# Performance work log

Measured on AMD Instinct MI355X. Metric: run time of the kernel, lower is better.

The kernel has to match this reference:

```python
import jax, jax.numpy as jnp
import numpy as np

B, N, D_IN, D_ATT = 8, 2048, 512, 512


def setup_inputs() -> dict:
    key = jax.random.key(0)
    ks = jax.random.split(key, 7)
    s_in = 1.0 / np.sqrt(D_IN)
    return {
        "x": jax.random.normal(ks[0], (B, N, D_IN), dtype=jnp.float32),
        "Wq": jax.random.uniform(ks[1], (D_IN, D_ATT), jnp.float32, -s_in, s_in),
        "bq": jax.random.uniform(ks[2], (D_ATT,), jnp.float32, -s_in, s_in),
        "Wk": jax.random.uniform(ks[3], (D_IN, D_ATT), jnp.float32, -s_in, s_in),
        "bk": jax.random.uniform(ks[4], (D_ATT,), jnp.float32, -s_in, s_in),
        "Wv": jax.random.uniform(ks[5], (D_IN, D_ATT), jnp.float32, -s_in, s_in),
        "bv": jax.random.uniform(ks[6], (D_ATT,), jnp.float32, -s_in, s_in),
    }


def reference(x, Wq, bq, Wk, bk, Wv, bv):
    # QKV projections: [B, N, D_ATT]
    Q = jnp.einsum("bnd,de->bne", x, Wq) + bq
    K = jnp.einsum("bnd,de->bne", x, Wk) + bk
    V = jnp.einsum("bnd,de->bne", x, Wv) + bv
    scale = 1.0 / jnp.sqrt(jnp.asarray(Q.shape[-1], Q.dtype))
    # scores[b, i, j] = Q[b,i] . K[b,j]  -> [B, N, N]
    scores = jnp.einsum("bie,bje->bij", Q, K) * scale
    # NOTE: original uses nn.Softmax(dim=1) -> normalize over the FIRST seq axis (queries)
    weights = jax.nn.softmax(scores, axis=1)
    out = jnp.einsum("bij,bje->bie", weights, V)
    return (out, weights)
```

## Files before the change

### kernel.cpp

```cpp
#include <hip/hip_runtime.h>
#include <hip/hip_bf16.h>
#include <stdint.h>

#define BB 8
#define NN 2048
#define DD 512

typedef unsigned short u16;
typedef __attribute__((ext_vector_type(8))) short bf16x8;
typedef __attribute__((ext_vector_type(8))) unsigned short u16x8;
typedef __attribute__((ext_vector_type(4))) float f32x4;

__device__ __forceinline__ float b2f(u16 h) {
  unsigned int u = ((unsigned int)h) << 16;
  float f;
  __builtin_memcpy(&f, &u, 4);
  return f;
}
__device__ __forceinline__ u16 f2b(float f) {
  unsigned int u;
  __builtin_memcpy(&u, &f, 4);
  u += 0x7fffu + ((u >> 16) & 1u);
  return (u16)(u >> 16);
}

__device__ __forceinline__ void glds16(const u16* g, u16* l) {
  __builtin_amdgcn_global_load_lds(
      (const __attribute__((address_space(1))) unsigned int*)g,
      (__attribute__((address_space(3))) unsigned int*)l, 16, 0, 0);
}

__global__ __launch_bounds__(256, 3)
void gemm_qkv(const u16* __restrict__ xb, const u16* __restrict__ WT,
              const float* __restrict__ bq, const float* __restrict__ bk,
              const float* __restrict__ bv,
              u16* __restrict__ Qb, u16* __restrict__ Kb, u16* __restrict__ VTb)
{
  __shared__ __align__(16) u16 sA[128 * 64];
  __shared__ __align__(16) u16 sB[128 * 64];
  const int tid  = threadIdx.x;
  const int wave = tid >> 6;
  const int lane = tid & 63;
  const int m0 = blockIdx.y * 128;
  const int n0 = blockIdx.x * 128;

  const int srow = wave * 8 + (lane >> 3);
  const int scol = (lane & 7) * 8;
  const u16* gA = xb + (long long)(m0 + srow) * 512 + scol;
  const u16* gB = WT + (long long)(n0 + srow) * 512 + scol;
  u16* lA = sA + wave * 512;
  u16* lB = sB + wave * 512;

  f32x4 acc[4][4];
#pragma unroll
  for (int i = 0; i < 4; ++i)
#pragma unroll
    for (int j = 0; j < 4; ++j) {
      f32x4 z = {0.f, 0.f, 0.f, 0.f};
      acc[i][j] = z;
    }

  const int wm  = (wave & 1) * 64;
  const int wn  = (wave >> 1) * 64;
  const int l15 = lane & 15;
  const int qk  = (lane >> 4) * 8;

  for (int k0 = 0; k0 < 512; k0 += 64) {
#pragma unroll
    for (int r = 0; r < 4; ++r) {
      glds16(gA + (long long)(r * 32) * 512 + k0, lA + r * 2048);
      glds16(gB + (long long)(r * 32) * 512 + k0, lB + r * 2048);
    }
    __syncthreads();
#pragma unroll
    for (int kk = 0; kk < 64; kk += 32) {
      bf16x8 af[4], bg[4];
#pragma unroll
      for (int mt = 0; mt < 4; ++mt)
        af[mt] = *(const bf16x8*)(sA + (wm + mt * 16 + l15) * 64 + kk + qk);
#pragma unroll
      for (int nt = 0; nt < 4; ++nt)
        bg[nt] = *(const bf16x8*)(sB + (wn + nt * 16 + l15) * 64 + kk + qk);
#pragma unroll
      for (int mt = 0; mt < 4; ++mt)
#pragma unroll
        for (int nt = 0; nt < 4; ++nt)
          acc[mt][nt] = __builtin_amdgcn_mfma_f32_16x16x32_bf16(
              af[mt], bg[nt], acc[mt][nt], 0, 0, 0);
    }
    __syncthreads();
  }

  const int rowq = (lane >> 4) * 4;
  const int route = n0 >> 9;
  const float* bp = (route == 0) ? bq : (route == 1) ? bk : bv;
#pragma unroll
  for (int nt = 0; nt < 4; ++nt) {
    const int gn = n0 + wn + nt * 16 + l15;
    const int ln = gn & 511;
    const float bval = bp[ln];
#pragma unroll
    for (int mt = 0; mt < 4; ++mt) {
      const int gm = m0 + wm + mt * 16 + rowq;
      if (route == 2) {
        const int b = gm >> 11;
        const int i = gm & (NN - 1);
        ushort4 pk;
        pk.x = f2b(acc[mt][nt][0] + bval);
        pk.y = f2b(acc[mt][nt][1] + bval);
        pk.z = f2b(acc[mt][nt][2] + bval);
        pk.w = f2b(acc[mt][nt][3] + bval);
        *(ushort4*)(&VTb[((long long)b * DD + ln) * NN + i]) = pk;
      } else {
        u16* Cb = (route == 0) ? Qb : Kb;
#pragma unroll
        for (int r = 0; r < 4; ++r)
          Cb[(long long)(gm + r) * DD + ln] = f2b(acc[mt][nt][r] + bval);
      }
    }
  }
}

__global__ __launch_bounds__(256, 3)
void gemm_s(const u16* __restrict__ Qb, const u16* __restrict__ Kb,
            u16* __restrict__ Eb, float* __restrict__ pl, float alpha)
{
  __shared__ __align__(16) u16 sA[128 * 64];
  __shared__ __align__(16) u16 sB[128 * 64];
  const int tid  = threadIdx.x;
  const int wave = tid >> 6;
  const int lane = tid & 63;
  const int m0 = blockIdx.y * 128;
  const int n0 = blockIdx.x * 128;
  const long long bz = blockIdx.z;
  const u16* A  = Qb + bz * (long long)NN * DD;
  const u16* Bt = Kb + bz * (long long)NN * DD;
  u16* E = Eb + bz * (long long)NN * NN;

  const int srow = wave * 8 + (lane >> 3);
  const int scol = (lane & 7) * 8;
  const u16* gA = A  + (long long)(m0 + srow) * DD + scol;
  const u16* gB = Bt + (long long)(n0 + srow) * DD + scol;
  u16* lA = sA + wave * 512;
  u16* lB = sB + wave * 512;

  f32x4 acc[4][4];
#pragma unroll
  for (int i = 0; i < 4; ++i)
#pragma unroll
    for (int j = 0; j < 4; ++j) {
      f32x4 z = {0.f, 0.f, 0.f, 0.f};
      acc[i][j] = z;
    }

  const int wm  = (wave & 1) * 64;
  const int wn  = (wave >> 1) * 64;
  const int l15 = lane & 15;
  const int qk  = (lane >> 4) * 8;

  for (int k0 = 0; k0 < DD; k0 += 64) {
#pragma unroll
    for (int r = 0; r < 4; ++r) {
      glds16(gA + (long long)(r * 32) * DD + k0, lA + r * 2048);
      glds16(gB + (long long)(r * 32) * DD + k0, lB + r * 2048);
    }
    __syncthreads();
#pragma unroll
    for (int kk = 0; kk < 64; kk += 32) {
      bf16x8 af[4], bg[4];
#pragma unroll
      for (int mt = 0; mt < 4; ++mt)
        af[mt] = *(const bf16x8*)(sA + (wm + mt * 16 + l15) * 64 + kk + qk);
#pragma unroll
      for (int nt = 0; nt < 4; ++nt)
        bg[nt] = *(const bf16x8*)(sB + (wn + nt * 16 + l15) * 64 + kk + qk);
#pragma unroll
      for (int mt = 0; mt < 4; ++mt)
#pragma unroll
        for (int nt = 0; nt < 4; ++nt)
          acc[mt][nt] = __builtin_amdgcn_mfma_f32_16x16x32_bf16(
              af[mt], bg[nt], acc[mt][nt], 0, 0, 0);
    }
    __syncthreads();
  }

  const int rowq = (lane >> 4) * 4;
  float coll[4];
#pragma unroll
  for (int nt = 0; nt < 4; ++nt) {
    float e[16];
#pragma unroll
    for (int mt = 0; mt < 4; ++mt)
#pragma unroll
      for (int r = 0; r < 4; ++r)
        e[mt * 4 + r] = __expf(fminf(acc[mt][nt][r] * alpha, 30.f));
    float sum = 0.f;
#pragma unroll
    for (int k = 0; k < 16; ++k) sum += e[k];
    sum += __shfl_xor(sum, 16);
    sum += __shfl_xor(sum, 32);
    coll[nt] = sum;
    const int gn = n0 + wn + nt * 16 + l15;
#pragma unroll
    for (int mt = 0; mt < 4; ++mt)
#pragma unroll
      for (int r = 0; r < 4; ++r)
        E[(long long)(m0 + wm + mt * 16 + rowq + r) * NN + gn] = f2b(e[mt * 4 + r]);
  }

  float* sred = (float*)sA;
  if (lane < 16) {
#pragma unroll
    for (int nt = 0; nt < 4; ++nt) {
      const int col = wn + nt * 16 + l15;
      sred[col * 2 + (wave & 1)] = coll[nt];
    }
  }
  __syncthreads();
  if (tid < 128) {
    const long long o = ((long long)bz * 16 + blockIdx.y) * NN + n0 + tid;
    pl[o] = sred[tid * 2] + sred[tid * 2 + 1];
  }
}

__global__ __launch_bounds__(256, 3)
void gemm_pv(const u16* __restrict__ A, const u16* __restrict__ Bt,
             float* __restrict__ C, int N, int K,
             long long sAb, long long sBb, long long sCb)
{
  __shared__ __align__(16) u16 sA[128 * 64];
  __shared__ __align__(16) u16 sB[128 * 64];
  const int tid  = threadIdx.x;
  const int wave = tid >> 6;
  const int lane = tid & 63;
  const int m0 = blockIdx.y * 128;
  const int n0 = blockIdx.x * 128;
  const long long bz = blockIdx.z;
  A  += bz * sAb;
  Bt += bz * sBb;
  C  += bz * sCb;

  const int srow = wave * 8 + (lane >> 3);
  const int scol = (lane & 7) * 8;
  const u16* gA = A  + (long long)(m0 + srow) * K + scol;
  const u16* gB = Bt + (long long)(n0 + srow) * K + scol;
  u16* lA = sA + wave * 512;
  u16* lB = sB + wave * 512;

  f32x4 acc[4][4];
#pragma unroll
  for (int i = 0; i < 4; ++i)
#pragma unroll
    for (int j = 0; j < 4; ++j) {
      f32x4 z = {0.f, 0.f, 0.f, 0.f};
      acc[i][j] = z;
    }

  const int wm  = (wave & 1) * 64;
  const int wn  = (wave >> 1) * 64;
  const int l15 = lane & 15;
  const int qk  = (lane >> 4) * 8;

  for (int k0 = 0; k0 < K; k0 += 64) {
#pragma unroll
    for (int r = 0; r < 4; ++r) {
      glds16(gA + (long long)(r * 32) * K + k0, lA + r * 2048);
      glds16(gB + (long long)(r * 32) * K + k0, lB + r * 2048);
    }
    __syncthreads();
#pragma unroll
    for (int kk = 0; kk < 64; kk += 32) {
      bf16x8 af[4], bg[4];
#pragma unroll
      for (int mt = 0; mt < 4; ++mt)
        af[mt] = *(const bf16x8*)(sA + (wm + mt * 16 + l15) * 64 + kk + qk);
#pragma unroll
      for (int nt = 0; nt < 4; ++nt)
        bg[nt] = *(const bf16x8*)(sB + (wn + nt * 16 + l15) * 64 + kk + qk);
#pragma unroll
      for (int mt = 0; mt < 4; ++mt)
#pragma unroll
        for (int nt = 0; nt < 4; ++nt)
          acc[mt][nt] = __builtin_amdgcn_mfma_f32_16x16x32_bf16(
              af[mt], bg[nt], acc[mt][nt], 0, 0, 0);
    }
    __syncthreads();
  }

  const int rowq = (lane >> 4) * 4;
#pragma unroll
  for (int nt = 0; nt < 4; ++nt) {
    const int gn = n0 + wn + nt * 16 + l15;
#pragma unroll
    for (int mt = 0; mt < 4; ++mt) {
#pragma unroll
      for (int r = 0; r < 4; ++r) {
        const int gm = m0 + wm + mt * 16 + rowq + r;
        C[(long long)gm * N + gn] = acc[mt][nt][r];
      }
    }
  }
}

__global__ __launch_bounds__(256)
void prep_inputs(const float* __restrict__ x, u16* __restrict__ xb,
                 const float* __restrict__ w0, const float* __restrict__ w1,
                 const float* __restrict__ w2, u16* __restrict__ WT)
{
  __shared__ float tile[64][65];
  const int bx = blockIdx.x;
  if (bx < 8192) {
    const long long i = ((long long)bx * 256 + threadIdx.x) * 4;
    const float4 v = *(const float4*)(x + i);
    ushort4 o;
    o.x = f2b(v.x); o.y = f2b(v.y); o.z = f2b(v.z); o.w = f2b(v.w);
    *(ushort4*)(xb + i) = o;
    return;
  }
  const int t = bx - 8192;
  const int z = t >> 6;
  const int s = t & 63;
  const float* in = (z == 0) ? w0 : (z == 1) ? w1 : w2;
  u16* o = WT + (long long)z * 512 * 512;
  const int r0 = (s >> 3) * 64;
  const int c0 = (s & 7) * 64;
  const int tr = threadIdx.x >> 6;
  const int tc = threadIdx.x & 63;
#pragma unroll
  for (int k = 0; k < 16; ++k) {
    const int r = k * 4 + tr;
    tile[r][tc] = in[(long long)(r0 + r) * 512 + c0 + tc];
  }
  __syncthreads();
#pragma unroll
  for (int k = 0; k < 16; ++k) {
    const int r = k * 4 + tr;
    o[(long long)(c0 + r) * 512 + r0 + tc] = f2b(tile[tc][r]);
  }
}

__global__ __launch_bounds__(256)
void softmax_combine(const float* __restrict__ pl, float* __restrict__ ec)
{
  const int idx = blockIdx.x * 256 + threadIdx.x;
  const int b = idx >> 11;
  const int j = idx & (NN - 1);
  const float* bl = pl + (long long)b * 16 * NN + j;
  float l = 0.f;
#pragma unroll
  for (int t = 0; t < 16; ++t)
    l += bl[(long long)t * NN];
  ec[idx] = 1.0f / l;
}

__global__ __launch_bounds__(256)
void vscale(u16* __restrict__ VTb, const float* __restrict__ ec)
{
  const long long idx = ((long long)blockIdx.x * 256 + threadIdx.x) * 8;
  const int b  = (int)(idx >> 20);
  const int j0 = (int)(idx & (NN - 1));
  const float* e = ec + b * NN + j0;
  u16x8 v = *(const u16x8*)(VTb + idx);
  u16x8 o;
#pragma unroll
  for (int k = 0; k < 8; ++k) o[k] = f2b(b2f(v[k]) * e[k]);
  *(u16x8*)(VTb + idx) = o;
}

__global__ __launch_bounds__(256)
void softmax_normalize(const u16* __restrict__ Eb, float* __restrict__ Wf,
                       const float* __restrict__ ec)
{
  const long long idx = ((long long)blockIdx.x * 256 + threadIdx.x) * 8;
  const int b  = (int)(idx >> 22);
  const int j0 = (int)(idx & (NN - 1));
  const float* e = ec + b * NN + j0;
  u16x8 v = *(const u16x8*)(Eb + idx);
  float w[8];
#pragma unroll
  for (int k = 0; k < 8; ++k)
    w[k] = b2f(v[k]) * e[k];
  float4 o0 = {w[0], w[1], w[2], w[3]};
  float4 o1 = {w[4], w[5], w[6], w[7]};
  *(float4*)(Wf + idx)     = o0;
  *(float4*)(Wf + idx + 4) = o1;
}

extern "C" void kernel_launch(void* const* d_in, const int* in_sizes, int n_in,
                              void* d_out, int out_size, void* d_ws, size_t ws_size,
                              hipStream_t stream)
{
  const float* x  = (const float*)d_in[0];
  const float* Wq = (const float*)d_in[1];
  const float* bq = (const float*)d_in[2];
  const float* Wk = (const float*)d_in[3];
  const float* bk = (const float*)d_in[4];
  const float* Wv = (const float*)d_in[5];
  const float* bv = (const float*)d_in[6];

  float* outf = (float*)d_out;
  float* Wf   = outf + (long long)BB * NN * DD;

  u16* Qb = (u16*)d_out;
  u16* Kb = Qb + (long long)BB * NN * DD;

  u16* Eb  = (u16*)d_ws;
  u16* spare = Eb + (long long)BB * NN * NN;
  u16* VTb = spare + (long long)BB * NN * NN;
  u16* xb  = VTb + (long long)BB * NN * DD;
  u16* WT  = xb + (long long)BB * NN * DD;
  float* pl  = (float*)(WT + 1536 * 512);
  float* ec  = pl + (long long)8 * 16 * NN;

  dim3 blk(256);

  prep_inputs<<<dim3(8192 + 192), blk, 0, stream>>>(x, xb, Wq, Wk, Wv, WT);

  gemm_qkv<<<dim3(12, 128), blk, 0, stream>>>(xb, WT, bq, bk, bv, Qb, Kb, VTb);

  const float scale = 0.044194173824159216f;
  gemm_s<<<dim3(16, 16, 8), blk, 0, stream>>>(Qb, Kb, Eb, pl, scale);

  softmax_combine<<<dim3(64), blk, 0, stream>>>(pl, ec);
  vscale<<<dim3(4096), blk, 0, stream>>>(VTb, ec);
  softmax_normalize<<<dim3(16384), blk, 0, stream>>>(Eb, Wf, ec);

  gemm_pv<<<dim3(4, 16, 8), blk, 0, stream>>>(Eb, VTb, outf, DD, NN,
      (long long)NN * NN, (long long)DD * NN, (long long)NN * DD);
}
```

Before: 363.0 us.

## Merge softmax normalization into PV GEMM launch as extra blocks

Removes the separate softmax_normalize kernel and folds its work into the PV GEMM launch. The grid grows from 4 to 12 blocks in x: the first 4 do the GEMM and the other 8 each normalize 32768 bf16 weights into the fp32 output. The memory-bound normalize can then run alongside the compute-bound GEMM and one launch is saved. In exchange, the GEMM blocks compete with the streaming blocks for bandwidth and CU slots, and both still read the same Eb buffer.

```diff
diff --git a/kernel.cpp b/kernel.cpp
--- a/kernel.cpp
+++ b/kernel.cpp
@@ -224,26 +224,51 @@
 }
 
 __global__ __launch_bounds__(256, 3)
-void gemm_pv(const u16* __restrict__ A, const u16* __restrict__ Bt,
-             float* __restrict__ C, int N, int K,
-             long long sAb, long long sBb, long long sCb)
+void gemm_pv_norm(const u16* __restrict__ A, const u16* __restrict__ Bt,
+                  float* __restrict__ C, float* __restrict__ Wf,
+                  const float* __restrict__ ec, int N, int K,
+                  long long sAb, long long sBb, long long sCb)
 {
   __shared__ __align__(16) u16 sA[128 * 64];
   __shared__ __align__(16) u16 sB[128 * 64];
-  const int tid  = threadIdx.x;
+  const int bx  = blockIdx.x;
+  const int tid = threadIdx.x;
+
+  if (bx >= 4) {
+    const int nb = (bx - 4) + 8 * (blockIdx.y + 16 * (int)blockIdx.z);
+    const long long base = (long long)nb * 32768;
+#pragma unroll
+    for (int it = 0; it < 16; ++it) {
+      const long long idx = base + it * 2048 + tid * 8;
+      const int b  = (int)(idx >> 22);
+      const int j0 = (int)(idx & (NN - 1));
+      const float* c = ec + b * NN + j0;
+      u16x8 v = *(const u16x8*)(A + idx);
+      float w[8];
+#pragma unroll
+      for (int k = 0; k < 8; ++k)
+        w[k] = b2f(v[k]) * c[k];
+      float4 o0 = {w[0], w[1], w[2], w[3]};
+      float4 o1 = {w[4], w[5], w[6], w[7]};
+      *(float4*)(Wf + idx)     = o0;
+      *(float4*)(Wf + idx + 4) = o1;
+    }
+    return;
+  }
+
   const int wave = tid >> 6;
   const int lane = tid & 63;
   const int m0 = blockIdx.y * 128;
-  const int n0 = blockIdx.x * 128;
+  const int n0 = bx * 128;
   const long long bz = blockIdx.z;
-  A  += bz * sAb;
-  Bt += bz * sBb;
-  C  += bz * sCb;
+  const u16* Ab  = A  + bz * sAb;
+  const u16* Btb = Bt + bz * sBb;
+  float* Cb      = C  + bz * sCb;
 
   const int srow = wave * 8 + (lane >> 3);
   const int scol = (lane & 7) * 8;
-  const u16* gA = A  + (long long)(m0 + srow) * K + scol;
-  const u16* gB = Bt + (long long)(n0 + srow) * K + scol;
+  const u16* gA = Ab  + (long long)(m0 + srow) * K + scol;
+  const u16* gB = Btb + (long long)(n0 + srow) * K + scol;
   u16* lA = sA + wave * 512;
   u16* lB = sB + wave * 512;
 
@@ -296,7 +321,7 @@
 #pragma unroll
       for (int r = 0; r < 4; ++r) {
         const int gm = m0 + wm + mt * 16 + rowq + r;
-        C[(long long)gm * N + gn] = acc[mt][nt][r];
+        Cb[(long long)gm * N + gn] = acc[mt][nt][r];
       }
     }
   }
@@ -367,25 +392,6 @@
   *(u16x8*)(VTb + idx) = o;
 }
 
-__global__ __launch_bounds__(256)
-void softmax_normalize(const u16* __restrict__ Eb, float* __restrict__ Wf,
-                       const float* __restrict__ ec)
-{
-  const long long idx = ((long long)blockIdx.x * 256 + threadIdx.x) * 8;
-  const int b  = (int)(idx >> 22);
-  const int j0 = (int)(idx & (NN - 1));
-  const float* e = ec + b * NN + j0;
-  u16x8 v = *(const u16x8*)(Eb + idx);
-  float w[8];
-#pragma unroll
-  for (int k = 0; k < 8; ++k)
-    w[k] = b2f(v[k]) * e[k];
-  float4 o0 = {w[0], w[1], w[2], w[3]};
-  float4 o1 = {w[4], w[5], w[6], w[7]};
-  *(float4*)(Wf + idx)     = o0;
-  *(float4*)(Wf + idx + 4) = o1;
-}
-
 extern "C" void kernel_launch(void* const* d_in, const int* in_sizes, int n_in,
                               void* d_out, int out_size, void* d_ws, size_t ws_size,
                               hipStream_t stream)
@@ -423,8 +429,7 @@
 
   softmax_combine<<<dim3(64), blk, 0, stream>>>(pl, ec);
   vscale<<<dim3(4096), blk, 0, stream>>>(VTb, ec);
-  softmax_normalize<<<dim3(16384), blk, 0, stream>>>(Eb, Wf, ec);
-
-  gemm_pv<<<dim3(4, 16, 8), blk, 0, stream>>>(Eb, VTb, outf, DD, NN,
-      (long long)NN * NN, (long long)DD * NN, (long long)NN * DD);
-}
+
+  gemm_pv_norm<<<dim3(12, 16, 8), blk, 0, stream>>>(Eb, VTb, outf, Wf, ec,
+      DD, NN, (long long)NN * NN, (long long)DD * NN, (long long)NN * DD);
+}
```

Result: slower. 380.9 us (+4.9%).
